# Kernel optimization log

Measured on AMD Instinct MI355X. Metric: run time of the kernel, lower is better.

Reference implementation:

```python
import jax, jax.numpy as jnp
import numpy as np

TOKENS, IN_F, OUT_F = 8192, 4096, 4096

def setup_inputs() -> dict:
    key = jax.random.key(0)
    k1, k2, k3, k4 = jax.random.split(key, 4)
    # int8 activations and weights in [-127, 127]
    x = jax.random.randint(k1, (TOKENS, IN_F), -127, 128, dtype=jnp.int32).astype(jnp.int8)
    weight = jax.random.randint(k2, (OUT_F, IN_F), -127, 128, dtype=jnp.int32).astype(jnp.int8)  # [out, in]
    # static per-output-channel dequant scale (fp16), small so fp16 output doesn't overflow
    dequant_scale = (jax.random.uniform(k3, (OUT_F,), dtype=jnp.float32) * 1e-3).astype(jnp.float16)
    bias = (jax.random.normal(k4, (OUT_F,), dtype=jnp.float32)).astype(jnp.float16)
    return {"x": x, "weight": weight, "dequant_scale": dequant_scale, "bias": bias}

def reference(x, weight, dequant_scale, bias):
    # int8 GEMM with int32 accumulation: [tokens, in] @ [in, out] -> [tokens, out]
    acc = jax.lax.dot_general(
        x, weight.T,
        dimension_numbers=(((1,), (0,)), ((), ())),
        preferred_element_type=jnp.int32,
    )
    # static per-output-channel dequant, cast to fp16, add fp16 bias
    out = (acc.astype(jnp.float32) * dequant_scale.astype(jnp.float32)[None, :]).astype(jnp.float16)
    out = out + bias[None, :]
    # module returns (output, output_bias)
    return (out, bias)
```

## Files before the change

kernel.cpp:

```cpp
#include <hip/hip_runtime.h>
#include <hip/hip_fp16.h>
#include <stdint.h>

typedef __attribute__((ext_vector_type(4))) int int32x4;
typedef __attribute__((ext_vector_type(4))) float float32x4;

#define TOKENS 8192
#define IN_F   4096
#define OUT_F  4096
#define BM 256
#define BN 256
#define BK 128
#define NT (IN_F / BK)
#define ESTR 260

__global__ __launch_bounds__(256)
void pack_all_kernel(const int* __restrict__ x32, const int* __restrict__ w32,
                     const float* __restrict__ bias,
                     uint32_t* __restrict__ x8, uint32_t* __restrict__ w8,
                     float* __restrict__ bias_out)
{
    const int gid = blockIdx.x * 256 + threadIdx.x;
    if (gid < OUT_F / 4)
        ((float32x4*)bias_out)[gid] = ((const float32x4*)bias)[gid];

    const int nx4 = TOKENS * IN_F / 4;
    const int nw4 = OUT_F * IN_F / 4;
    for (int i = gid; i < nx4 + nw4; i += gridDim.x * 256) {
        const int* s; uint32_t* d; int j;
        if (i < nx4) { s = x32; d = x8; j = i; }
        else         { s = w32; d = w8; j = i - nx4; }
        int32x4 v = ((const int32x4*)s)[j];
        d[j] = (uint32_t)(v[0] & 0xff) | ((uint32_t)(v[1] & 0xff) << 8) |
               ((uint32_t)(v[2] & 0xff) << 16) | ((uint32_t)v[3] << 24);
    }
}

__global__ __launch_bounds__(512, 2)
void w8a8_gemm_kernel(const int8_t* __restrict__ x,
                      const int8_t* __restrict__ w,
                      const float* __restrict__ scale,
                      const float* __restrict__ bias,
                      float* __restrict__ out)
{
    __shared__ int8_t smem[131072];
    int8_t* lA = smem;
    int8_t* lB = smem + 65536;

    const int tid = threadIdx.x;
    const int wv  = tid >> 6;
    const int l   = tid & 63;
    const int wqm = wv >> 1;
    const int wqn = wv & 1;

    const int bn = blockIdx.x;
    const int bm = blockIdx.y;

    const int8_t* baseA = x + (size_t)bm * BM * IN_F;
    const int8_t* baseB = w + (size_t)bn * BN * IN_F;

    const int seg0 = wv * 2, seg1 = wv * 2 + 1;
    const int r8   = l >> 3;
    const int swc  = (((l & 7) ^ r8) << 4);

    const int8_t* pA0 = baseA + (size_t)(seg0 * 8 + r8) * IN_F + swc;
    const int8_t* pA1 = baseA + (size_t)(seg1 * 8 + r8) * IN_F + swc;
    const int8_t* pB0 = baseB + (size_t)(seg0 * 8 + r8) * IN_F + swc;
    const int8_t* pB1 = baseB + (size_t)(seg1 * 8 + r8) * IN_F + swc;

    const int fr  = l & 15;
    const int xk  = (l & 7) << 4;
    const int cb0 = (l >> 4) << 4;

    int32x4 acc[2][2][2][4];
#pragma unroll
    for (int a0 = 0; a0 < 2; ++a0)
#pragma unroll
        for (int a1 = 0; a1 < 2; ++a1)
#pragma unroll
            for (int a2 = 0; a2 < 2; ++a2)
#pragma unroll
                for (int a3 = 0; a3 < 4; ++a3)
                    acc[a0][a1][a2][a3] = (int32x4){0, 0, 0, 0};

    int32x4 aF[2][2];
    int32x4 bF0[4][2];
    int32x4 bF1[4][2];

    auto stage_half = [&](int h4) {
        const int kt_ = h4 >> 2;
        const int wh_ = h4 & 3;
        const size_t off = (size_t)(wh_ & 1) * (128 * IN_F) + (size_t)kt_ * BK;
        const int8_t* s0 = ((wh_ < 2) ? pA0 : pB0) + off;
        const int8_t* s1 = ((wh_ < 2) ? pA1 : pB1) + off;
        int8_t* db = ((wh_ < 2) ? lA : lB) + ((kt_ & 1) << 15) + ((wh_ & 1) << 14);
        __builtin_amdgcn_global_load_lds(
            (const __attribute__((address_space(1))) void*)s0,
            (__attribute__((address_space(3))) void*)(db + seg0 * 1024), 16, 0, 0);
        __builtin_amdgcn_global_load_lds(
            (const __attribute__((address_space(1))) void*)s1,
            (__attribute__((address_space(3))) void*)(db + seg1 * 1024), 16, 0, 0);
    };

#define LDA(MH)                                                                        \
    do {                                                                               \
        _Pragma("unroll") for (int mi = 0; mi < 2; ++mi)                               \
        _Pragma("unroll") for (int ks = 0; ks < 2; ++ks)                               \
            aF[mi][ks] = *(const int32x4*)&lAb[((MH) << 14) +                          \
                (wqm * 32 + mi * 16 + fr) * 128 + (((ks * 64) + cb0) ^ xk)];           \
    } while (0)

#define LDB(NH, DST)                                                                   \
    do {                                                                               \
        _Pragma("unroll") for (int ni = 0; ni < 4; ++ni)                               \
        _Pragma("unroll") for (int ks = 0; ks < 2; ++ks)                               \
            DST[ni][ks] = *(const int32x4*)&lBb[((NH) << 14) +                         \
                (wqn * 64 + ni * 16 + fr) * 128 + (((ks * 64) + cb0) ^ xk)];           \
    } while (0)

#define MMAQ(MH, NH, BF)                                                               \
    do {                                                                               \
        _Pragma("unroll") for (int mi = 0; mi < 2; ++mi)                               \
        _Pragma("unroll") for (int ni = 0; ni < 4; ++ni)                               \
        _Pragma("unroll") for (int ks = 0; ks < 2; ++ks)                               \
            acc[MH][NH][mi][ni] = __builtin_amdgcn_mfma_i32_16x16x64_i8(               \
                aF[mi][ks], BF[ni][ks], acc[MH][NH][mi][ni], 0, 0, 0);                 \
    } while (0)

    stage_half(0); stage_half(1); stage_half(2); stage_half(3);
    stage_half(4);
    asm volatile("s_waitcnt vmcnt(2)" ::: "memory");
    __builtin_amdgcn_s_barrier();

    for (int t = 0; t < NT; ++t) {
        const int8_t* lAb = lA + ((t & 1) << 15);
        const int8_t* lBb = lB + ((t & 1) << 15);

        LDA(0); LDB(0, bF0); LDB(1, bF1);
        if (t + 1 < NT) {
            stage_half(4 * (t + 1) + 1);
            stage_half(4 * (t + 1) + 2);
            stage_half(4 * (t + 1) + 3);
        }
        __builtin_amdgcn_s_barrier();
        asm volatile("s_waitcnt lgkmcnt(0)" ::: "memory");
        __builtin_amdgcn_s_setprio(1);
        MMAQ(0, 0, bF0); MMAQ(0, 1, bF1);
        __builtin_amdgcn_s_setprio(0);
        __builtin_amdgcn_s_barrier();

        LDA(1);
        if (t + 2 < NT) stage_half(4 * (t + 2) + 0);
        if (t + 2 < NT)      asm volatile("s_waitcnt vmcnt(2)" ::: "memory");
        else if (t + 1 < NT) asm volatile("s_waitcnt vmcnt(0)" ::: "memory");
        __builtin_amdgcn_s_barrier();
        asm volatile("s_waitcnt lgkmcnt(0)" ::: "memory");
        __builtin_amdgcn_s_setprio(1);
        MMAQ(1, 0, bF0); MMAQ(1, 1, bF1);
        __builtin_amdgcn_s_setprio(0);
        __builtin_amdgcn_s_barrier();
    }

    __syncthreads();
    int* eL = (int*)smem;
    const int c4   = tid & 63;
    const int rowt = tid >> 6;
    const float32x4 sc4 = ((const float32x4*)scale)[bn * 64 + c4];
    const float32x4 bf4 = ((const float32x4*)bias )[bn * 64 + c4];
    const __half bh[4] = { __float2half(bf4[0]), __float2half(bf4[1]),
                           __float2half(bf4[2]), __float2half(bf4[3]) };
    const int r0 = (l >> 4) << 2;
    const int wr0 = (wqm & 1) * 32 + r0;

    for (int c = 0; c < 4; ++c) {
        if ((wqm >> 1) == (c & 1)) {
            const int MH = c >> 1;
#pragma unroll
            for (int NH = 0; NH < 2; ++NH)
#pragma unroll
                for (int mi = 0; mi < 2; ++mi)
#pragma unroll
                    for (int ni = 0; ni < 4; ++ni)
#pragma unroll
                        for (int r = 0; r < 4; ++r)
                            eL[(wr0 + mi * 16 + r) * ESTR +
                               NH * 128 + wqn * 64 + ni * 16 + fr] = acc[MH][NH][mi][ni][r];
        }
        __syncthreads();
#pragma unroll
        for (int p = 0; p < 8; ++p) {
            const int rl = p * 8 + rowt;
            int32x4 v = *(const int32x4*)&eL[rl * ESTR + c4 * 4];
            float32x4 o;
#pragma unroll
            for (int j = 0; j < 4; ++j) {
                __half h = __float2half((float)v[j] * sc4[j]);
                o[j] = __half2float(__hadd(h, bh[j]));
            }
            const size_t rowg = (size_t)(bm * 256 + c * 64 + rl);
            ((float32x4*)out)[rowg * (OUT_F / 4) + bn * 64 + c4] = o;
        }
        __syncthreads();
    }
#undef LDA
#undef LDB
#undef MMAQ
}

extern "C" void kernel_launch(void* const* d_in, const int* in_sizes, int n_in,
                              void* d_out, int out_size, void* d_ws, size_t ws_size,
                              hipStream_t stream)
{
    const int*   x32   = (const int*)d_in[0];
    const int*   w32   = (const int*)d_in[1];
    const float* scale = (const float*)d_in[2];
    const float* bias  = (const float*)d_in[3];
    float* out = (float*)d_out;

    int8_t* x8 = (int8_t*)d_ws;
    int8_t* w8 = x8 + (size_t)TOKENS * IN_F;

    pack_all_kernel<<<3072, 256, 0, stream>>>(x32, w32, bias, (uint32_t*)x8, (uint32_t*)w8,
                                              out + (size_t)TOKENS * OUT_F);

    dim3 grid(OUT_F / BN, TOKENS / BM);
    w8a8_gemm_kernel<<<grid, 512, 0, stream>>>(x8, w8, scale, bias, out);
}
```

Before: 196.5 us.

## Use 4-stage BK=64 LDS pipeline with remapped block order for L2 locality

Reduces the K tile from 128 to 64 and replaces the double-buffered half-stage scheme with a 4-deep ring of LDS buffers, prefetching three steps ahead with one barrier-separated MFMA phase per step. It removes the XOR swizzle in LDS addressing and uses a 1D grid with remapping that groups blocks into 8x8 tiles spread across XCD-like groups, to improve L2 reuse. The unswizzled 64-byte row layout may cause LDS bank conflicts on fragment reads. Halving BK also doubles the number of loop iterations and barriers.

```diff
diff --git a/kernel.cpp b/kernel.cpp
--- a/kernel.cpp
+++ b/kernel.cpp
@@ -10,9 +10,12 @@
 #define OUT_F  4096
 #define BM 256
 #define BN 256
-#define BK 128
-#define NT (IN_F / BK)
+#define BK 64
+#define NSTEP (IN_F / BK)
 #define ESTR 260
+
+#define AS1 __attribute__((address_space(1)))
+#define AS3 __attribute__((address_space(3)))
 
 __global__ __launch_bounds__(256)
 void pack_all_kernel(const int* __restrict__ x32, const int* __restrict__ w32,
@@ -53,23 +56,23 @@
     const int wqm = wv >> 1;
     const int wqn = wv & 1;
 
-    const int bn = blockIdx.x;
-    const int bm = blockIdx.y;
+    const int xc  = blockIdx.x & 7;
+    const int idx = blockIdx.x >> 3;
+    const int bn  = (xc & 1) * 8 + (idx & 7);
+    const int bm  = (xc >> 1) * 8 + (idx >> 3);
 
     const int8_t* baseA = x + (size_t)bm * BM * IN_F;
     const int8_t* baseB = w + (size_t)bn * BN * IN_F;
 
-    const int seg0 = wv * 2, seg1 = wv * 2 + 1;
-    const int r8   = l >> 3;
-    const int swc  = (((l & 7) ^ r8) << 4);
-
-    const int8_t* pA0 = baseA + (size_t)(seg0 * 8 + r8) * IN_F + swc;
-    const int8_t* pA1 = baseA + (size_t)(seg1 * 8 + r8) * IN_F + swc;
-    const int8_t* pB0 = baseB + (size_t)(seg0 * 8 + r8) * IN_F + swc;
-    const int8_t* pB1 = baseB + (size_t)(seg1 * 8 + r8) * IN_F + swc;
+    const int   srow  = tid >> 2;
+    const int   sbyte = (tid & 3) << 4;
+    const int8_t* pA0 = baseA + (size_t)srow * IN_F + sbyte;
+    const int8_t* pA1 = baseA + (size_t)(srow + 128) * IN_F + sbyte;
+    const int8_t* pB0 = baseB + (size_t)srow * IN_F + sbyte;
+    const int8_t* pB1 = baseB + (size_t)(srow + 128) * IN_F + sbyte;
+    const int   dofs  = tid << 4;
 
     const int fr  = l & 15;
-    const int xk  = (l & 7) << 4;
     const int cb0 = (l >> 4) << 4;
 
     int32x4 acc[2][2][2][4];
@@ -84,79 +87,61 @@
                     acc[a0][a1][a2][a3] = (int32x4){0, 0, 0, 0};
 
     int32x4 aF[2][2];
-    int32x4 bF0[4][2];
-    int32x4 bF1[4][2];
-
-    auto stage_half = [&](int h4) {
-        const int kt_ = h4 >> 2;
-        const int wh_ = h4 & 3;
-        const size_t off = (size_t)(wh_ & 1) * (128 * IN_F) + (size_t)kt_ * BK;
-        const int8_t* s0 = ((wh_ < 2) ? pA0 : pB0) + off;
-        const int8_t* s1 = ((wh_ < 2) ? pA1 : pB1) + off;
-        int8_t* db = ((wh_ < 2) ? lA : lB) + ((kt_ & 1) << 15) + ((wh_ & 1) << 14);
-        __builtin_amdgcn_global_load_lds(
-            (const __attribute__((address_space(1))) void*)s0,
-            (__attribute__((address_space(3))) void*)(db + seg0 * 1024), 16, 0, 0);
-        __builtin_amdgcn_global_load_lds(
-            (const __attribute__((address_space(1))) void*)s1,
-            (__attribute__((address_space(3))) void*)(db + seg1 * 1024), 16, 0, 0);
+    int32x4 bF[2][4];
+
+    auto stage_step = [&](int t) {
+        const int b = t & 3;
+        int8_t* dA = lA + b * 16384;
+        int8_t* dB = lB + b * 16384;
+        const size_t co = (size_t)t * BK;
+        __builtin_amdgcn_global_load_lds((const AS1 void*)(pA0 + co),
+                                         (AS3 void*)(dA + dofs), 16, 0, 0);
+        __builtin_amdgcn_global_load_lds((const AS1 void*)(pA1 + co),
+                                         (AS3 void*)(dA + 8192 + dofs), 16, 0, 0);
+        __builtin_amdgcn_global_load_lds((const AS1 void*)(pB0 + co),
+                                         (AS3 void*)(dB + dofs), 16, 0, 0);
+        __builtin_amdgcn_global_load_lds((const AS1 void*)(pB1 + co),
+                                         (AS3 void*)(dB + 8192 + dofs), 16, 0, 0);
     };
 
-#define LDA(MH)                                                                        \
-    do {                                                                               \
-        _Pragma("unroll") for (int mi = 0; mi < 2; ++mi)                               \
-        _Pragma("unroll") for (int ks = 0; ks < 2; ++ks)                               \
-            aF[mi][ks] = *(const int32x4*)&lAb[((MH) << 14) +                          \
-                (wqm * 32 + mi * 16 + fr) * 128 + (((ks * 64) + cb0) ^ xk)];           \
-    } while (0)
-
-#define LDB(NH, DST)                                                                   \
-    do {                                                                               \
-        _Pragma("unroll") for (int ni = 0; ni < 4; ++ni)                               \
-        _Pragma("unroll") for (int ks = 0; ks < 2; ++ks)                               \
-            DST[ni][ks] = *(const int32x4*)&lBb[((NH) << 14) +                         \
-                (wqn * 64 + ni * 16 + fr) * 128 + (((ks * 64) + cb0) ^ xk)];           \
-    } while (0)
-
-#define MMAQ(MH, NH, BF)                                                               \
-    do {                                                                               \
-        _Pragma("unroll") for (int mi = 0; mi < 2; ++mi)                               \
-        _Pragma("unroll") for (int ni = 0; ni < 4; ++ni)                               \
-        _Pragma("unroll") for (int ks = 0; ks < 2; ++ks)                               \
-            acc[MH][NH][mi][ni] = __builtin_amdgcn_mfma_i32_16x16x64_i8(               \
-                aF[mi][ks], BF[ni][ks], acc[MH][NH][mi][ni], 0, 0, 0);                 \
-    } while (0)
-
-    stage_half(0); stage_half(1); stage_half(2); stage_half(3);
-    stage_half(4);
-    asm volatile("s_waitcnt vmcnt(2)" ::: "memory");
+    stage_step(0); stage_step(1); stage_step(2);
+    asm volatile("s_waitcnt vmcnt(8)" ::: "memory");
     __builtin_amdgcn_s_barrier();
 
-    for (int t = 0; t < NT; ++t) {
-        const int8_t* lAb = lA + ((t & 1) << 15);
-        const int8_t* lBb = lB + ((t & 1) << 15);
-
-        LDA(0); LDB(0, bF0); LDB(1, bF1);
-        if (t + 1 < NT) {
-            stage_half(4 * (t + 1) + 1);
-            stage_half(4 * (t + 1) + 2);
-            stage_half(4 * (t + 1) + 3);
-        }
+    for (int t = 0; t < NSTEP; ++t) {
+        const int8_t* lAb = lA + (t & 3) * 16384;
+        const int8_t* lBb = lB + (t & 3) * 16384;
+
+#pragma unroll
+        for (int MH = 0; MH < 2; ++MH)
+#pragma unroll
+            for (int mi = 0; mi < 2; ++mi)
+                aF[MH][mi] = *(const int32x4*)&lAb[(MH * 128 + wqm * 32 + mi * 16 + fr) * 64 + cb0];
+#pragma unroll
+        for (int NH = 0; NH < 2; ++NH)
+#pragma unroll
+            for (int ni = 0; ni < 4; ++ni)
+                bF[NH][ni] = *(const int32x4*)&lBb[(NH * 128 + wqn * 64 + ni * 16 + fr) * 64 + cb0];
+
+        if (t + 3 < NSTEP) stage_step(t + 3);
+
+        if (t + 3 < NSTEP)      asm volatile("s_waitcnt vmcnt(8)" ::: "memory");
+        else if (t + 2 < NSTEP) asm volatile("s_waitcnt vmcnt(4)" ::: "memory");
+        else if (t + 1 < NSTEP) asm volatile("s_waitcnt vmcnt(0)" ::: "memory");
+
         __builtin_amdgcn_s_barrier();
         asm volatile("s_waitcnt lgkmcnt(0)" ::: "memory");
         __builtin_amdgcn_s_setprio(1);
-        MMAQ(0, 0, bF0); MMAQ(0, 1, bF1);
-        __builtin_amdgcn_s_setprio(0);
-        __builtin_amdgcn_s_barrier();
-
-        LDA(1);
-        if (t + 2 < NT) stage_half(4 * (t + 2) + 0);
-        if (t + 2 < NT)      asm volatile("s_waitcnt vmcnt(2)" ::: "memory");
-        else if (t + 1 < NT) asm volatile("s_waitcnt vmcnt(0)" ::: "memory");
-        __builtin_amdgcn_s_barrier();
-        asm volatile("s_waitcnt lgkmcnt(0)" ::: "memory");
-        __builtin_amdgcn_s_setprio(1);
-        MMAQ(1, 0, bF0); MMAQ(1, 1, bF1);
+#pragma unroll
+        for (int MH = 0; MH < 2; ++MH)
+#pragma unroll
+            for (int NH = 0; NH < 2; ++NH)
+#pragma unroll
+                for (int mi = 0; mi < 2; ++mi)
+#pragma unroll
+                    for (int ni = 0; ni < 4; ++ni)
+                        acc[MH][NH][mi][ni] = __builtin_amdgcn_mfma_i32_16x16x64_i8(
+                            aF[MH][mi], bF[NH][ni], acc[MH][NH][mi][ni], 0, 0, 0);
         __builtin_amdgcn_s_setprio(0);
         __builtin_amdgcn_s_barrier();
     }
@@ -202,9 +187,6 @@
         }
         __syncthreads();
     }
-#undef LDA
-#undef LDB
-#undef MMAQ
 }
 
 extern "C" void kernel_launch(void* const* d_in, const int* in_sizes, int n_in,
@@ -223,6 +205,5 @@
     pack_all_kernel<<<3072, 256, 0, stream>>>(x32, w32, bias, (uint32_t*)x8, (uint32_t*)w8,
                                               out + (size_t)TOKENS * OUT_F);
 
-    dim3 grid(OUT_F / BN, TOKENS / BM);
-    w8a8_gemm_kernel<<<grid, 512, 0, stream>>>(x8, w8, scale, bias, out);
+    w8a8_gemm_kernel<<<512, 512, 0, stream>>>(x8, w8, scale, bias, out);
 }
```

Result: slower. 210.7 us (+7.3%).
